# Performance work log

Hardware: AMD Instinct MI355X
Metric: run time of the kernel (lower is better)

## Reference

```python
import jax, jax.numpy as jnp
from jax import lax
import numpy as np

P = 16      # n_latent
T = 16      # n_frames
ALPHA = 0.5


def conv2d(x, w, b):
    # Conv2d(k=3, stride=2, pad=1), NCHW/OIHW
    y = lax.conv_general_dilated(x, w, (2, 2), ((1, 1), (1, 1)),
                                 dimension_numbers=('NCHW', 'OIHW', 'NCHW'))
    return y + b[None, :, None, None]


def convT2d(x, w, b):
    # ConvTranspose2d(k=3, stride=2, pad=1, output_pad=1): lhs_dilation=2,
    # pad low = k-1-p = 1, pad high = k-1-p+op = 2, kernel flipped, I/O swapped.
    wk = jnp.flip(w, (2, 3)).transpose(1, 0, 2, 3)
    y = lax.conv_general_dilated(x, wk, (1, 1), ((1, 2), (1, 2)),
                                 lhs_dilation=(2, 2),
                                 dimension_numbers=('NCHW', 'OIHW', 'NCHW'))
    return y + b[None, :, None, None]


def build_tridiag(D, Boff, alpha):
    # D: [B, P*P*T], Boff: [B, P*P*(T-1)] -> block-tridiagonal [B, P*T, P*T]
    b = D.shape[0]
    Db = D.reshape(b, T, P, P)
    Bb = Boff.reshape(b, T - 1, P, P)
    blocks = jnp.zeros((b, T, T, P, P), D.dtype)
    i = jnp.arange(T)
    blocks = blocks.at[:, i, i].set(Db)                                # diagonal blocks
    blocks = blocks.at[:, i[1:], i[:-1]].set(Bb)                        # sub-diagonal
    blocks = blocks.at[:, i[:-1], i[1:]].set(Bb.transpose(0, 1, 3, 2))  # super-diagonal (transposed)
    M = blocks.transpose(0, 1, 3, 2, 4).reshape(b, P * T, P * T)
    return M + alpha * jnp.eye(P * T, dtype=D.dtype)


def setup_inputs() -> dict:
    key = jax.random.key(0)
    ks = jax.random.split(key, 20)
    B = 256

    def kaiming(k, shape, fan_in):
        return jax.random.normal(k, shape, jnp.float32) * np.float32(np.sqrt(2.0 / fan_in))

    inp = {}
    inp['x'] = jax.random.normal(ks[0], (B, T, 32, 32), jnp.float32)
    inp['eps'] = jax.random.normal(ks[1], (B, P * T), jnp.float32)
    # encoder convs
    inp['w1'] = kaiming(ks[2], (32, 1, 3, 3), 9);     inp['b1'] = jnp.zeros((32,), jnp.float32)
    inp['w2'] = kaiming(ks[3], (32, 32, 3, 3), 288);  inp['b2'] = jnp.zeros((32,), jnp.float32)
    inp['w3'] = kaiming(ks[4], (64, 32, 3, 3), 288);  inp['b3'] = jnp.zeros((64,), jnp.float32)
    inp['w4'] = kaiming(ks[5], (64, 64, 3, 3), 576);  inp['b4'] = jnp.zeros((64,), jnp.float32)
    inp['w5'] = kaiming(ks[6], (64, 64, 3, 3), 576);  inp['b5'] = jnp.zeros((64,), jnp.float32)
    # encoder fc heads
    F = 64 * T
    inp['fc_mu_w'] = kaiming(ks[7], (P * T, F), F);   inp['fc_mu_b'] = jnp.zeros((P * T,), jnp.float32)
    # tiny std so alpha*I dominates -> precision matrix is PD (valid Cholesky)
    inp['fc_D_w'] = jax.random.normal(ks[8], (P * P * T, F), jnp.float32) * np.float32(3e-5)
    inp['fc_D_b'] = jnp.zeros((P * P * T,), jnp.float32)
    inp['fc_B_w'] = jax.random.normal(ks[9], (P * P * (T - 1), F), jnp.float32) * np.float32(3e-5)
    inp['fc_B_b'] = jnp.zeros((P * P * (T - 1),), jnp.float32)
    # decoder
    inp['fc_dec_w'] = kaiming(ks[10], (F, P * T), P * T); inp['fc_dec_b'] = jnp.zeros((F,), jnp.float32)
    inp['wt5'] = kaiming(ks[11], (64, 64, 3, 3), 576); inp['bt5'] = jnp.zeros((64,), jnp.float32)
    inp['wt4'] = kaiming(ks[12], (64, 64, 3, 3), 576); inp['bt4'] = jnp.zeros((64,), jnp.float32)
    inp['wt3'] = kaiming(ks[13], (64, 32, 3, 3), 576); inp['bt3'] = jnp.zeros((32,), jnp.float32)
    inp['wt2'] = kaiming(ks[14], (32, 32, 3, 3), 288); inp['bt2'] = jnp.zeros((32,), jnp.float32)
    inp['wt1'] = kaiming(ks[15], (32, 1, 3, 3), 288);  inp['bt1'] = jnp.zeros((1,), jnp.float32)
    return inp


def reference(x, eps, w1, b1, w2, b2, w3, b3, w4, b4, w5, b5,
              fc_mu_w, fc_mu_b, fc_D_w, fc_D_b, fc_B_w, fc_B_b,
              fc_dec_w, fc_dec_b, wt5, bt5, wt4, bt4, wt3, bt3,
              wt2, bt2, wt1, bt1):
    Bsz = x.shape[0]
    # ---- encode ----
    h = x.reshape(-1, 1, 32, 32)
    for w, b in ((w1, b1), (w2, b2), (w3, b3), (w4, b4), (w5, b5)):
        h = jax.nn.relu(conv2d(h, w, b))      # ends at [B*T, 64, 1, 1]
    h = h.reshape(Bsz, 64 * T)
    mu = h @ fc_mu_w.T + fc_mu_b              # [B, P*T]
    Dv = h @ fc_D_w.T + fc_D_b                # [B, P*P*T]
    Bv = h @ fc_B_w.T + fc_B_b                # [B, P*P*(T-1)]
    # ---- reparametrize ----
    Pm = build_tridiag(Dv, Bv, ALPHA)         # [B, P*T, P*T]
    L = jnp.linalg.cholesky(Pm)               # lower, uses lower triangle (as torch.cholesky)
    cov = jnp.linalg.inv(L)                   # per-sample inverse of Cholesky factor
    z = mu + jnp.einsum('bij,bj->bi', cov, eps)
    # ---- decode ----
    hd = (z @ fc_dec_w.T + fc_dec_b).reshape(-1, 64, 1, 1)
    for w, b in ((wt5, bt5), (wt4, bt4), (wt3, bt3), (wt2, bt2)):
        hd = jax.nn.elu(convT2d(hd, w, b))
    xr = jax.nn.sigmoid(convT2d(hd, wt1, bt1))  # [B*T, 1, 32, 32]
    return (xr, mu, cov, Pm)
```

## Files before the change

### kernel.cpp

```cpp
#include <hip/hip_runtime.h>
#include <cmath>

#define ALPHA 0.5f

__global__ __launch_bounds__(256) void transpose_all8(
    const float* __restrict__ dw5, const float* __restrict__ dw4,
    const float* __restrict__ dw3, const float* __restrict__ dw2,
    const float* __restrict__ ew2, const float* __restrict__ ew3,
    const float* __restrict__ ew4, const float* __restrict__ ew5,
    float* __restrict__ t5, float* __restrict__ t4,
    float* __restrict__ t3, float* __restrict__ t2,
    float* __restrict__ e2, float* __restrict__ e3,
    float* __restrict__ e4, float* __restrict__ e5)
{
    int idx = blockIdx.x * 256 + threadIdx.x;
    if (idx >= 202752) return;
    const float* w; float* t; int CIN, COUT, loc; bool enc = false;
    if (idx < 36864)       { w = dw5; t = t5; CIN = 64; COUT = 64; loc = idx; }
    else if (idx < 73728)  { w = dw4; t = t4; CIN = 64; COUT = 64; loc = idx - 36864; }
    else if (idx < 92160)  { w = dw3; t = t3; CIN = 64; COUT = 32; loc = idx - 73728; }
    else if (idx < 101376) { w = dw2; t = t2; CIN = 32; COUT = 32; loc = idx - 92160; }
    else if (idx < 110592) { w = ew2; t = e2; CIN = 32; COUT = 32; loc = idx - 101376; enc = true; }
    else if (idx < 129024) { w = ew3; t = e3; CIN = 32; COUT = 64; loc = idx - 110592; enc = true; }
    else if (idx < 165888) { w = ew4; t = e4; CIN = 64; COUT = 64; loc = idx - 129024; enc = true; }
    else                   { w = ew5; t = e5; CIN = 64; COUT = 64; loc = idx - 165888; enc = true; }
    int wk = loc % 9; int r = loc / 9; int ci, co;
    if (enc) { ci = r % CIN;  co = r / CIN;  }
    else     { co = r % COUT; ci = r / COUT; }
    t[wk * CIN * COUT + ci * COUT + co] = w[loc];
}

__device__ __forceinline__ int a1map(int iy, int col) {
    return (col & 7)
         | ((iy & 2) << 2)
         | (((iy ^ (iy >> 2)) & 1) << 4)
         | ((col & 8) << 2)
         | ((iy & 4) << 4)
         | ((iy & 8) << 4);
}

__global__ __launch_bounds__(256, 4) void enc_fused(
    const float* __restrict__ x,
    const float* __restrict__ w1,  const float* __restrict__ b1,
    const float* __restrict__ w2t, const float* __restrict__ b2,
    const float* __restrict__ w3t, const float* __restrict__ b3,
    const float* __restrict__ w4t, const float* __restrict__ b4,
    const float* __restrict__ w5t, const float* __restrict__ b5,
    float* __restrict__ hout)
{
    __shared__ __align__(16) float smem[10240];
    float* a1s  = smem;
    float* bse  = smem + 8192;
    float* imgs = bse;
    float* a2s  = bse;
    float* a3s  = smem;
    float* a4s  = smem + 1024;
    float* reds = smem + 1280;

    const int n = blockIdx.x;
    const int tid = threadIdx.x;

    const float* xi = x + n * 1024;
    #pragma unroll
    for (int i = 0; i < 4; i++) {
        int idx = tid + 256 * i;
        int iy = idx >> 5, ix = idx & 31;
        int col = (ix & 1) ? 20 + (ix >> 1) : (ix >> 1);
        imgs[iy * 40 + col] = xi[idx];
    }
    __syncthreads();

    {
        const int oy = tid >> 4, ox = tid & 15;
        float patch[9];
        #pragma unroll
        for (int ky = 0; ky < 3; ky++) {
            const int iy = 2 * oy - 1 + ky;
            #pragma unroll
            for (int kx = 0; kx < 3; kx++) {
                const int ix = 2 * ox - 1 + kx;
                bool v = (iy >= 0) && (ix >= 0);
                int col = (ix & 1) ? 20 + (ix >> 1) : (ix >> 1);
                patch[ky * 3 + kx] = v ? imgs[iy * 40 + col] : 0.f;
            }
        }
        const int ocol = (ox & 1) ? 8 + (ox >> 1) : (ox >> 1);
        const int sidx = a1map(oy, ocol);
        for (int c = 0; c < 32; c++) {
            float acc = b1[c];
            #pragma unroll
            for (int k = 0; k < 9; k++) acc = fmaf(patch[k], w1[c * 9 + k], acc);
            a1s[c * 256 + sidx] = fmaxf(acc, 0.f);
        }
    }
    __syncthreads();

    {
        const int p = tid & 63, oy = p >> 3, ox = p & 7;
        const int c0u = __builtin_amdgcn_readfirstlane(tid >> 6);
        const int cobase = c0u * 8;
        float acc[8];
        #pragma unroll
        for (int r = 0; r < 8; r++) acc[r] = b2[cobase + r];
        int offs[9]; bool val[9];
        #pragma unroll
        for (int ky = 0; ky < 3; ky++) {
            const int iy = 2 * oy - 1 + ky;
            #pragma unroll
            for (int kx = 0; kx < 3; kx++) {
                const int ix = 2 * ox - 1 + kx;
                const bool v = (iy >= 0) && (ix >= 0);
                const int col = (ix & 1) ? 8 + (ix >> 1) : (ix >> 1);
                offs[ky * 3 + kx] = v ? a1map(iy, col) : 0;
                val[ky * 3 + kx] = v;
            }
        }
        for (int ci = 0; ci < 32; ci++) {
            float patch[9];
            #pragma unroll
            for (int k = 0; k < 9; k++)
                patch[k] = val[k] ? a1s[ci * 256 + offs[k]] : 0.f;
            const float* wci = w2t + ci * 32 + cobase;
            #pragma unroll
            for (int k = 0; k < 9; k++) {
                #pragma unroll
                for (int r = 0; r < 8; r++)
                    acc[r] = fmaf(patch[k], wci[k * 1024 + r], acc[r]);
            }
        }
        __syncthreads();
        #pragma unroll
        for (int r = 0; r < 8; r++)
            a2s[(cobase + r) * 64 + p] = fmaxf(acc[r], 0.f);
    }
    __syncthreads();

    {
        const int px = tid & 15, oy = px >> 2, ox = px & 3;
        const int cg = tid >> 4;
        float4 bv = ((const float4*)b3)[cg];
        float acc[4] = {bv.x, bv.y, bv.z, bv.w};
        for (int ci = 0; ci < 32; ci++) {
            float patch[9];
            #pragma unroll
            for (int ky = 0; ky < 3; ky++) {
                const int iy = 2 * oy - 1 + ky;
                #pragma unroll
                for (int kx = 0; kx < 3; kx++) {
                    const int ix = 2 * ox - 1 + kx;
                    bool v = (iy >= 0) && (ix >= 0);
                    patch[ky * 3 + kx] = v ? a2s[ci * 64 + iy * 8 + ix] : 0.f;
                }
            }
            #pragma unroll
            for (int k = 0; k < 9; k++) {
                float4 wv = *(const float4*)(w3t + k * 2048 + ci * 64 + cg * 4);
                acc[0] = fmaf(patch[k], wv.x, acc[0]);
                acc[1] = fmaf(patch[k], wv.y, acc[1]);
                acc[2] = fmaf(patch[k], wv.z, acc[2]);
                acc[3] = fmaf(patch[k], wv.w, acc[3]);
            }
        }
        #pragma unroll
        for (int r = 0; r < 4; r++)
            a3s[(cg * 4 + r) * 16 + px] = fmaxf(acc[r], 0.f);
    }
    __syncthreads();

    {
        const int co = tid & 63;
        const int part = __builtin_amdgcn_readfirstlane(tid >> 6);
        float a0 = 0.f, a1 = 0.f, a2 = 0.f, a3 = 0.f;
        for (int ci = part * 16; ci < part * 16 + 16; ci++) {
            const float* wp = w4t + ci * 64 + co;
            const float w0 = wp[0];
            const float w1 = wp[4096];
            const float w2 = wp[8192];
            const float w3 = wp[12288];
            const float w4 = wp[16384];
            const float w5 = wp[20480];
            const float w6 = wp[24576];
            const float w7 = wp[28672];
            const float w8 = wp[32768];
            const float4 r0 = *(const float4*)(a3s + ci * 16);
            const float4 r1 = *(const float4*)(a3s + ci * 16 + 4);
            const float4 r2 = *(const float4*)(a3s + ci * 16 + 8);
            const float4 r3 = *(const float4*)(a3s + ci * 16 + 12);
            a0 = fmaf(r0.x, w4, a0); a0 = fmaf(r0.y, w5, a0);
            a0 = fmaf(r1.x, w7, a0); a0 = fmaf(r1.y, w8, a0);
            a1 = fmaf(r0.y, w3, a1); a1 = fmaf(r0.z, w4, a1); a1 = fmaf(r0.w, w5, a1);
            a1 = fmaf(r1.y, w6, a1); a1 = fmaf(r1.z, w7, a1); a1 = fmaf(r1.w, w8, a1);
            a2 = fmaf(r1.x, w1, a2); a2 = fmaf(r1.y, w2, a2);
            a2 = fmaf(r2.x, w4, a2); a2 = fmaf(r2.y, w5, a2);
            a2 = fmaf(r3.x, w7, a2); a2 = fmaf(r3.y, w8, a2);
            a3 = fmaf(r1.y, w0, a3); a3 = fmaf(r1.z, w1, a3); a3 = fmaf(r1.w, w2, a3);
            a3 = fmaf(r2.y, w3, a3); a3 = fmaf(r2.z, w4, a3); a3 = fmaf(r2.w, w5, a3);
            a3 = fmaf(r3.y, w6, a3); a3 = fmaf(r3.z, w7, a3); a3 = fmaf(r3.w, w8, a3);
        }
        float* reds2 = bse;
        reds2[part * 256 +   0 + co] = a0;
        reds2[part * 256 +  64 + co] = a1;
        reds2[part * 256 + 128 + co] = a2;
        reds2[part * 256 + 192 + co] = a3;
        __syncthreads();
        {
            const int co2 = tid & 63;
            const int cls2 = __builtin_amdgcn_readfirstlane(tid >> 6);
            float s = b4[co2]
                    + reds2[      cls2 * 64 + co2] + reds2[256 + cls2 * 64 + co2]
                    + reds2[512 + cls2 * 64 + co2] + reds2[768 + cls2 * 64 + co2];
            a4s[co2 * 4 + cls2] = fmaxf(s, 0.f);
        }
    }
    __syncthreads();

    {
        const int c = tid & 63, part = tid >> 6;
        float s = 0.f;
        for (int ci = part * 16; ci < part * 16 + 16; ci++) {
            const float4 av = *(const float4*)(a4s + ci * 4);
            s = fmaf(av.x, w5t[4 * 4096 + ci * 64 + c], s);
            s = fmaf(av.y, w5t[5 * 4096 + ci * 64 + c], s);
            s = fmaf(av.z, w5t[7 * 4096 + ci * 64 + c], s);
            s = fmaf(av.w, w5t[8 * 4096 + ci * 64 + c], s);
        }
        reds[part * 64 + c] = s;
    }
    __syncthreads();
    if (tid < 64) {
        float v = b5[tid] + reds[tid] + reds[64 + tid] + reds[128 + tid] + reds[192 + tid];
        hout[n * 64 + tid] = fmaxf(v, 0.f);
    }
}

__global__ __launch_bounds__(256) void pm_zero(float4* __restrict__ Pm4)
{
    Pm4[blockIdx.x * 256 + threadIdx.x] = make_float4(0.f, 0.f, 0.f, 0.f);
}

__global__ __launch_bounds__(256) void fc_enc(
    const float* __restrict__ h,
    const float* __restrict__ wmu, const float* __restrict__ bmu,
    const float* __restrict__ wD,  const float* __restrict__ bD,
    const float* __restrict__ wB,  const float* __restrict__ bB,
    float* __restrict__ mu, float* __restrict__ Pm)
{
    __shared__ float As[32][65];
    __shared__ float Bs[32][65];
    const int tid = threadIdx.x;
    const int m0 = blockIdx.y * 64;
    const int n0 = blockIdx.x * 64;

    const float* wbase; const float* bias; int nloc; int region;
    if (n0 < 256)       { wbase = wmu; bias = bmu; nloc = n0;        region = 0; }
    else if (n0 < 4352) { wbase = wD;  bias = bD;  nloc = n0 - 256;  region = 1; }
    else                { wbase = wB;  bias = bB;  nloc = n0 - 4352; region = 2; }

    const int tx = tid & 15, ty = tid >> 4;
    float acc[4][4] = {};
    for (int k0 = 0; k0 < 1024; k0 += 32) {
        #pragma unroll
        for (int s = 0; s < 8; s++) {
            int l = tid + 256 * s;
            int row = l >> 5, kk = l & 31;
            As[kk][row] = h[(m0 + row) * 1024 + k0 + kk];
            Bs[kk][row] = wbase[(nloc + row) * 1024 + k0 + kk];
        }
        __syncthreads();
        #pragma unroll
        for (int kk = 0; kk < 32; kk++) {
            float av[4], bv[4];
            #pragma unroll
            for (int i = 0; i < 4; i++) av[i] = As[kk][ty * 4 + i];
            #pragma unroll
            for (int j = 0; j < 4; j++) bv[j] = Bs[kk][tx * 4 + j];
            #pragma unroll
            for (int i = 0; i < 4; i++)
                #pragma unroll
                for (int j = 0; j < 4; j++) acc[i][j] = fmaf(av[i], bv[j], acc[i][j]);
        }
        __syncthreads();
    }
    #pragma unroll
    for (int i = 0; i < 4; i++) {
        int m = m0 + ty * 4 + i;
        size_t pbase = (size_t)m * 65536;
        #pragma unroll
        for (int j = 0; j < 4; j++) {
            int nc = nloc + tx * 4 + j;
            float v = acc[i][j] + bias[nc];
            if (region == 0) {
                mu[m * 256 + nc] = v;
            } else {
                int t = nc >> 8, pi = (nc >> 4) & 15, pj = nc & 15;
                if (region == 1) {
                    int row = t * 16 + pi, col = t * 16 + pj;
                    Pm[pbase + row * 256 + col] = v + (pi == pj ? ALPHA : 0.f);
                } else {
                    int row = (t + 1) * 16 + pi, col = t * 16 + pj;
                    Pm[pbase + row * 256 + col] = v;
                    Pm[pbase + col * 256 + row] = v;
                }
            }
        }
    }
}

__global__ __launch_bounds__(64) void chol_band(
    const float* __restrict__ Pm, float* __restrict__ Lb_g)
{
    __shared__ float Lb[256 * 32 + 32];
    __shared__ float Ds[4096];
    __shared__ float Bs2[3840];
    const int b = blockIdx.x, lane = threadIdx.x;
    const float* Pb = Pm + (size_t)b * 65536;
    for (int i = lane; i < 8224; i += 64) Lb[i] = 0.f;
    for (int i = lane; i < 4096; i += 64) {
        int t = i >> 8, r = (i >> 4) & 15, c = i & 15;
        Ds[i] = Pb[(t * 16 + r) * 256 + t * 16 + c];
    }
    for (int i = lane; i < 3840; i += 64) {
        int t = i >> 8, r = (i >> 4) & 15, c = i & 15;
        Bs2[i] = Pb[((t + 1) * 16 + r) * 256 + t * 16 + c];
    }
    __syncthreads();

    const int d = lane;
    for (int j = 0; j < 256; j++) {
        const int i = j + d;
        float s = 0.f;
        if (d < 32 && i < 256) {
            int bi = i >> 4, bj = j >> 4, pi = i & 15, pj = j & 15;
            float a;
            if (bi == bj)           a = Ds[bi * 256 + pi * 16 + pj];
            else if (bi == bj + 1)  a = Bs2[bj * 256 + pi * 16 + pj];
            else                    a = 0.f;

            float c[32], p[32];
            const float* cp = Lb + j * 32;
            #pragma unroll
            for (int q = 0; q < 8; q++)
                *(float4*)(c + 4 * q) = *(const float4*)(cp + 4 * q);
            const float* pp = Lb + i * 32 + d;
            #pragma unroll
            for (int m = 1; m < 32; m++) p[m] = pp[m];

            float s0 = 0.f, s1 = 0.f, s2 = 0.f, s3 = 0.f;
            #pragma unroll
            for (int m = 1; m <= 28; m += 4) {
                s0 = fmaf(p[m],     c[m],     s0);
                s1 = fmaf(p[m + 1], c[m + 1], s1);
                s2 = fmaf(p[m + 2], c[m + 2], s2);
                s3 = fmaf(p[m + 3], c[m + 3], s3);
            }
            s0 = fmaf(p[29], c[29], s0);
            s1 = fmaf(p[30], c[30], s1);
            s2 = fmaf(p[31], c[31], s2);
            s = a - ((s0 + s1) + (s2 + s3));
        }
        float diag = __shfl(s, 0);
        float Ljj = sqrtf(diag);
        if (d == 0)                  Lb[j * 32] = Ljj;
        else if (d < 32 && i < 256)  Lb[i * 32 + d] = s / Ljj;
        __syncthreads();
    }
    for (int i = lane; i < 8192; i += 64) Lb_g[b * 8192 + i] = Lb[i];
}

__global__ __launch_bounds__(256) void inv_band(
    const float* __restrict__ Lb_g, float* __restrict__ cov)
{
    __shared__ __align__(16) float Ls[8192];
    __shared__ float rs[256];
    const int b = blockIdx.x, j = threadIdx.x;
    float* covb = cov + (size_t)b * 65536;

    {
        const float4* src = (const float4*)(Lb_g + b * 8192);
        float4* dst = (float4*)Ls;
        #pragma unroll
        for (int q = 0; q < 8; q++) dst[j + 256 * q] = src[j + 256 * q];
    }
    __syncthreads();
    rs[j] = 1.f / Ls[j * 32];
    __syncthreads();

    const int w = __builtin_amdgcn_readfirstlane(j >> 6);
    const int istart = w * 64;

    for (int i = 0; i < istart; i++) covb[i * 256 + j] = 0.f;

    float g[32];
    #pragma unroll
    for (int q = 0; q < 32; q++) g[q] = 0.f;

    for (int c = istart; c < 256; c += 32) {
        #pragma unroll
        for (int u = 0; u < 32; u++) {
            const int i = c + u;
            const float* Lr = Ls + i * 32;
            float s0 = 0.f, s1 = 0.f, s2 = 0.f, s3 = 0.f;
            #pragma unroll
            for (int d = 1; d < 32; d += 4) {
                s0 = fmaf(Lr[d],     g[(u - d) & 31],     s0);
                if (d + 1 < 32) s1 = fmaf(Lr[d + 1], g[(u - d - 1) & 31], s1);
                if (d + 2 < 32) s2 = fmaf(Lr[d + 2], g[(u - d - 2) & 31], s2);
                if (d + 3 < 32) s3 = fmaf(Lr[d + 3], g[(u - d - 3) & 31], s3);
            }
            float s = (s0 + s1) + (s2 + s3);
            float gi = (((i == j) ? 1.f : 0.f) - s) * rs[i];
            g[u & 31] = gi;
            covb[i * 256 + j] = gi;
        }
    }
}

__global__ __launch_bounds__(256) void zvec_k(
    const float* __restrict__ cov, const float* __restrict__ mu,
    const float* __restrict__ eps, float* __restrict__ z)
{
    __shared__ float es[256];
    const int b = blockIdx.x, i = threadIdx.x;
    es[i] = eps[b * 256 + i];
    __syncthreads();
    const float4* row = (const float4*)(cov + (size_t)b * 65536 + i * 256);
    float s = 0.f;
    #pragma unroll 8
    for (int k = 0; k < 64; k++) {
        float4 v = row[k];
        s = fmaf(v.x, es[4 * k], s);
        s = fmaf(v.y, es[4 * k + 1], s);
        s = fmaf(v.z, es[4 * k + 2], s);
        s = fmaf(v.w, es[4 * k + 3], s);
    }
    z[b * 256 + i] = mu[b * 256 + i] + s;
}

__global__ __launch_bounds__(256) void fc_dec_k(
    const float* __restrict__ z, const float* __restrict__ w,
    const float* __restrict__ bias, float* __restrict__ hd0)
{
    __shared__ float zs[256];
    const int blk = blockIdx.x;
    const int b = blk >> 2;
    const int f = ((blk & 3) << 8) + threadIdx.x;
    zs[threadIdx.x] = z[b * 256 + threadIdx.x];
    __syncthreads();
    const float4* wr = (const float4*)(w + f * 256);
    float s = 0.f;
    #pragma unroll 8
    for (int k = 0; k < 64; k++) {
        float4 v = wr[k];
        s = fmaf(v.x, zs[4 * k], s);
        s = fmaf(v.y, zs[4 * k + 1], s);
        s = fmaf(v.z, zs[4 * k + 2], s);
        s = fmaf(v.w, zs[4 * k + 3], s);
    }
    hd0[b * 1024 + f] = s + bias[f];
}

__global__ __launch_bounds__(256) void mu_fix(
    const float* __restrict__ h, const float* __restrict__ w,
    const float* __restrict__ bias, float* __restrict__ mu)
{
    __shared__ float hs[1024];
    const int b = blockIdx.x, p = threadIdx.x;
    #pragma unroll
    for (int i = 0; i < 4; i++) hs[p + 256 * i] = h[b * 1024 + p + 256 * i];
    __syncthreads();
    const float4* wr = (const float4*)(w + p * 1024);
    float s = 0.f;
    #pragma unroll 8
    for (int k = 0; k < 256; k++) {
        float4 v = wr[k];
        s = fmaf(v.x, hs[4 * k], s);
        s = fmaf(v.y, hs[4 * k + 1], s);
        s = fmaf(v.z, hs[4 * k + 2], s);
        s = fmaf(v.w, hs[4 * k + 3], s);
    }
    mu[b * 256 + p] = s + bias[p];
}

__device__ __forceinline__ float eluf(float v) { return v > 0.f ? v : expf(v) - 1.f; }

template<int PY, int PX, int HIN, int WIN, class F>
__device__ __forceinline__ void for_taps(int ey, int ex, F&& f) {
    if (PY == 0) {
        if (PX == 0) { f(4, ey, ex, true); }
        else         { f(5, ey, ex, true); f(3, ey, ex + 1, ex + 1 < WIN); }
    } else {
        if (PX == 0) { f(7, ey, ex, true); f(1, ey + 1, ex, ey + 1 < HIN); }
        else {
            f(8, ey, ex, true);
            f(6, ey, ex + 1, ex + 1 < WIN);
            f(2, ey + 1, ex, ey + 1 < HIN);
            f(0, ey + 1, ex + 1, (ey + 1 < HIN) && (ex + 1 < WIN));
        }
    }
}

template<int OY>
__device__ __forceinline__ void t4_row(
    const float* __restrict__ wt4t, const float* __restrict__ bt4,
    const float* __restrict__ d1, float* __restrict__ d2, int co)
{
    float a0 = 0.f, a1 = 0.f, a2 = 0.f, a3 = 0.f;
    const float* wb = wt4t + co;
    for (int ci = 0; ci < 64; ci++) {
        const float* base = d1 + ci * 12;
        if (OY % 2 == 0) {
            float4 r = *(const float4*)(base + (OY / 2) * 4);
            float w10 = wb[3 * 4096 + ci * 64];
            float w11 = wb[4 * 4096 + ci * 64];
            float w12 = wb[5 * 4096 + ci * 64];
            a0 = fmaf(r.x, w11, a0);
            a1 = fmaf(r.x, w12, a1); a1 = fmaf(r.y, w10, a1);
            a2 = fmaf(r.y, w11, a2);
            a3 = fmaf(r.y, w12, a3); a3 = fmaf(r.z, w10, a3);
        } else {
            float4 ra = *(const float4*)(base + ((OY - 1) / 2) * 4);
            float4 rb = *(const float4*)(base + ((OY + 1) / 2) * 4);
            float w20 = wb[6 * 4096 + ci * 64], w21 = wb[7 * 4096 + ci * 64], w22 = wb[8 * 4096 + ci * 64];
            float w00 = wb[0 * 4096 + ci * 64], w01 = wb[1 * 4096 + ci * 64], w02 = wb[2 * 4096 + ci * 64];
            a0 = fmaf(ra.x, w21, a0); a0 = fmaf(rb.x, w01, a0);
            a1 = fmaf(ra.x, w22, a1); a1 = fmaf(ra.y, w20, a1);
            a1 = fmaf(rb.x, w02, a1); a1 = fmaf(rb.y, w00, a1);
            a2 = fmaf(ra.y, w21, a2); a2 = fmaf(rb.y, w01, a2);
            a3 = fmaf(ra.y, w22, a3); a3 = fmaf(ra.z, w20, a3);
            a3 = fmaf(rb.y, w02, a3); a3 = fmaf(rb.z, w00, a3);
        }
    }
    float b = bt4[co];
    float4 o = make_float4(eluf(a0 + b), eluf(a1 + b), eluf(a2 + b), eluf(a3 + b));
    *(float4*)(d2 + co * 44 + OY * 8) = o;
}

template<int M>
__device__ __forceinline__ void xrow(float* acc, const float* R, float w0, float w1, float w2)
{
    #pragma unroll
    for (int m = 0; m < M; m++) {
        acc[2 * m]     = fmaf(R[m], w1, acc[2 * m]);
        acc[2 * m + 1] = fmaf(R[m], w2, acc[2 * m + 1]);
        acc[2 * m + 1] = fmaf(R[m + 1], w0, acc[2 * m + 1]);
    }
}

__global__ __launch_bounds__(256, 4) void dec_fused(
    const float* __restrict__ hd0,
    const float* __restrict__ wt5t, const float* __restrict__ bt5,
    const float* __restrict__ wt4t, const float* __restrict__ bt4,
    const float* __restrict__ wt3t, const float* __restrict__ bt3,
    const float* __restrict__ wt2t, const float* __restrict__ bt2,
    const float* __restrict__ wt1,  const float* __restrict__ bt1,
    float* __restrict__ xr)
{
    __shared__ __align__(16) float smem[9664];
    float* d0  = smem;
    float* d1  = smem + 64;
    float* d2  = smem + 832;
    float* scr = smem + 3648;
    float* d3  = smem + 6208;
    float* d4  = smem;

    const int n = blockIdx.x, tid = threadIdx.x;

    for (int i = tid; i < 3584; i += 256) smem[64 + i] = 0.f;
    for (int i = tid; i < 3456; i += 256) d3[i] = 0.f;
    if (tid < 64) d0[tid] = hd0[n * 64 + tid];
    __syncthreads();

    {
        const int co = tid & 63;
        const int wv = __builtin_amdgcn_readfirstlane(tid >> 6);
        const int oy = wv >> 1, ox = wv & 1;
        const int wk = (oy + 1) * 3 + (ox + 1);
        const float* wp = wt5t + wk * 4096 + co;
        float s = bt5[co];
        for (int ci = 0; ci < 64; ci++)
            s = fmaf(d0[ci], wp[ci * 64], s);
        d1[co * 12 + oy * 4 + ox] = eluf(s);
    }
    __syncthreads();

    {
        const int co = tid & 63;
        const int oyw = __builtin_amdgcn_readfirstlane(tid >> 6);
        if (oyw == 0)      t4_row<0>(wt4t, bt4, d1, d2, co);
        else if (oyw == 1) t4_row<1>(wt4t, bt4, d1, d2, co);
        else if (oyw == 2) t4_row<2>(wt4t, bt4, d1, d2, co);
        else               t4_row<3>(wt4t, bt4, d1, d2, co);
    }
    __syncthreads();

    {
        const int co = tid & 31, pr = (tid >> 5) & 3, cih = tid >> 7;
        const int e = (pr & 1) ? 7 - pr : pr;
        const int o = (pr & 1) ? pr : 7 - pr;
        const int iy_e = e >> 1, iy_o2 = (o - 1) >> 1, iy_o0 = (o + 1) >> 1;
        float acce[8] = {}, acco[8] = {};
        const float* wb = wt3t + co;
        for (int c = 0; c < 32; c++) {
            const int ci = cih * 32 + c;
            const float* base = d2 + ci * 44;
            float re[8], ro2[8], ro0[8];
            *(float4*)(re)      = *(const float4*)(base + iy_e * 8);
            *(float4*)(re + 4)  = *(const float4*)(base + iy_e * 8 + 4);
            *(float4*)(ro2)     = *(const float4*)(base + iy_o2 * 8);
            *(float4*)(ro2 + 4) = *(const float4*)(base + iy_o2 * 8 + 4);
            *(float4*)(ro0)     = *(const float4*)(base + iy_o0 * 8);
            *(float4*)(ro0 + 4) = *(const float4*)(base + iy_o0 * 8 + 4);
            float w10 = wb[3 * 2048 + ci * 32], w11 = wb[4 * 2048 + ci * 32], w12 = wb[5 * 2048 + ci * 32];
            float w20 = wb[6 * 2048 + ci * 32], w21 = wb[7 * 2048 + ci * 32], w22 = wb[8 * 2048 + ci * 32];
            float w00 = wb[0 * 2048 + ci * 32], w01 = wb[1 * 2048 + ci * 32], w02 = wb[2 * 2048 + ci * 32];
            xrow<4>(acce, re, w10, w11, w12);
            xrow<4>(acco, ro2, w20, w21, w22);
            xrow<4>(acco, ro0, w00, w01, w02);
        }
        if (cih == 1) {
            float* s = scr + (tid - 128) * 20;
            #pragma unroll
            for (int k = 0; k < 8; k++) { s[k] = acce[k]; s[8 + k] = acco[k]; }
        }
        __syncthreads();
        if (cih == 0) {
            const float* s = scr + tid * 20;
            const float b = bt3[co];
            float* oe = d3 + co * 108 + e * 12;
            float* oo = d3 + co * 108 + o * 12;
            #pragma unroll
            for (int k = 0; k < 8; k++) {
                oe[k] = eluf(acce[k] + s[k] + b);
                oo[k] = eluf(acco[k] + s[8 + k] + b);
            }
        }
    }
    __syncthreads();

    {
        const int co = tid & 31, org = tid >> 5;
        float acc0[16] = {}, acc1[16] = {};
        const float* wb = wt2t + co;
        for (int ci = 0; ci < 32; ci++) {
            const float* base = d3 + ci * 108 + org * 12;
            float A[12], B[12];
            #pragma unroll
            for (int q = 0; q < 3; q++) {
                *(float4*)(A + 4 * q) = *(const float4*)(base + 4 * q);
                *(float4*)(B + 4 * q) = *(const float4*)(base + 12 + 4 * q);
            }
            float w10 = wb[3 * 1024 + ci * 32], w11 = wb[4 * 1024 + ci * 32], w12 = wb[5 * 1024 + ci * 32];
            float w20 = wb[6 * 1024 + ci * 32], w21 = wb[7 * 1024 + ci * 32], w22 = wb[8 * 1024 + ci * 32];
            float w00 = wb[0 * 1024 + ci * 32], w01 = wb[1 * 1024 + ci * 32], w02 = wb[2 * 1024 + ci * 32];
            xrow<8>(acc0, A, w10, w11, w12);
            xrow<8>(acc1, A, w20, w21, w22);
            xrow<8>(acc1, B, w00, w01, w02);
        }
        __syncthreads();
        const float b = bt2[co];
        float* o0 = d4 + co * 260 + (2 * org) * 16;
        float* o1 = o0 + 16;
        #pragma unroll
        for (int q = 0; q < 4; q++) {
            float4 v0 = make_float4(eluf(acc0[4 * q] + b), eluf(acc0[4 * q + 1] + b),
                                    eluf(acc0[4 * q + 2] + b), eluf(acc0[4 * q + 3] + b));
            float4 v1 = make_float4(eluf(acc1[4 * q] + b), eluf(acc1[4 * q + 1] + b),
                                    eluf(acc1[4 * q + 2] + b), eluf(acc1[4 * q + 3] + b));
            *(float4*)(o0 + 4 * q) = v0;
            *(float4*)(o1 + 4 * q) = v1;
        }
    }
    __syncthreads();

    {
        const int ey = tid >> 4, ex = tid & 15;
        const float bb = bt1[0];
        float* xi = xr + n * 1024;
        float acc[4] = {};
        for (int ci = 0; ci < 32; ci++) {
            const float* a = d4 + ci * 260;
            const float* w = wt1 + ci * 9;
            for_taps<0, 0, 16, 16>(ey, ex, [&](int wk, int iy, int ix, bool v) {
                acc[0] = fmaf(v ? a[iy * 16 + ix] : 0.f, w[wk], acc[0]); });
            for_taps<0, 1, 16, 16>(ey, ex, [&](int wk, int iy, int ix, bool v) {
                acc[1] = fmaf(v ? a[iy * 16 + ix] : 0.f, w[wk], acc[1]); });
            for_taps<1, 0, 16, 16>(ey, ex, [&](int wk, int iy, int ix, bool v) {
                acc[2] = fmaf(v ? a[iy * 16 + ix] : 0.f, w[wk], acc[2]); });
            for_taps<1, 1, 16, 16>(ey, ex, [&](int wk, int iy, int ix, bool v) {
                acc[3] = fmaf(v ? a[iy * 16 + ix] : 0.f, w[wk], acc[3]); });
        }
        xi[(2 * ey) * 32 + 2 * ex]         = 1.f / (1.f + expf(-(acc[0] + bb)));
        xi[(2 * ey) * 32 + 2 * ex + 1]     = 1.f / (1.f + expf(-(acc[1] + bb)));
        xi[(2 * ey + 1) * 32 + 2 * ex]     = 1.f / (1.f + expf(-(acc[2] + bb)));
        xi[(2 * ey + 1) * 32 + 2 * ex + 1] = 1.f / (1.f + expf(-(acc[3] + bb)));
    }
}

extern "C" void kernel_launch(void* const* d_in, const int* in_sizes, int n_in,
                              void* d_out, int out_size, void* d_ws, size_t ws_size,
                              hipStream_t stream)
{
    (void)in_sizes; (void)n_in; (void)out_size; (void)ws_size;
    const float* x    = (const float*)d_in[0];
    const float* eps  = (const float*)d_in[1];
    const float* w1 = (const float*)d_in[2];  const float* b1 = (const float*)d_in[3];
    const float* w2 = (const float*)d_in[4];  const float* b2 = (const float*)d_in[5];
    const float* w3 = (const float*)d_in[6];  const float* b3 = (const float*)d_in[7];
    const float* w4 = (const float*)d_in[8];  const float* b4 = (const float*)d_in[9];
    const float* w5 = (const float*)d_in[10]; const float* b5 = (const float*)d_in[11];
    const float* fc_mu_w = (const float*)d_in[12]; const float* fc_mu_b = (const float*)d_in[13];
    const float* fc_D_w  = (const float*)d_in[14]; const float* fc_D_b  = (const float*)d_in[15];
    const float* fc_B_w  = (const float*)d_in[16]; const float* fc_B_b  = (const float*)d_in[17];
    const float* fc_dec_w = (const float*)d_in[18]; const float* fc_dec_b = (const float*)d_in[19];
    const float* wt5 = (const float*)d_in[20]; const float* bt5 = (const float*)d_in[21];
    const float* wt4 = (const float*)d_in[22]; const float* bt4 = (const float*)d_in[23];
    const float* wt3 = (const float*)d_in[24]; const float* bt3 = (const float*)d_in[25];
    const float* wt2 = (const float*)d_in[26]; const float* bt2 = (const float*)d_in[27];
    const float* wt1 = (const float*)d_in[28]; const float* bt1 = (const float*)d_in[29];

    float* ws   = (float*)d_ws;
    float* h    = ws;
    float* Lb   = ws + 262144;
    float* z    = ws + 2359296;
    float* hd0  = ws + 2424832;
    float* wt5t = ws + 2686976;
    float* wt4t = ws + 2723840;
    float* wt3t = ws + 2760704;
    float* wt2t = ws + 2779136;
    float* w2t  = ws + 2788352;
    float* w3t  = ws + 2797568;
    float* w4t  = ws + 2816000;
    float* w5t  = ws + 2852864;

    float* out = (float*)d_out;
    float* xr  = out;
    float* mu  = out + 4194304;
    float* cov = out + 4259840;
    float* Pm  = out + 21037056;

    transpose_all8<<<792, 256, 0, stream>>>(wt5, wt4, wt3, wt2, w2, w3, w4, w5,
                                            wt5t, wt4t, wt3t, wt2t, w2t, w3t, w4t, w5t);
    enc_fused<<<4096, 256, 0, stream>>>(x, w1, b1, w2t, b2, w3t, b3, w4t, b4, w5t, b5, h);
    pm_zero<<<16384, 256, 0, stream>>>((float4*)Pm);
    fc_enc<<<dim3(128, 4), 256, 0, stream>>>(h, fc_mu_w, fc_mu_b, fc_D_w, fc_D_b,
                                             fc_B_w, fc_B_b, mu, Pm);
    chol_band<<<256, 64, 0, stream>>>(Pm, Lb);
    inv_band<<<256, 256, 0, stream>>>(Lb, cov);
    zvec_k<<<256, 256, 0, stream>>>(cov, mu, eps, z);
    fc_dec_k<<<1024, 256, 0, stream>>>(z, fc_dec_w, fc_dec_b, hd0);
    dec_fused<<<4096, 256, 0, stream>>>(hd0, wt5t, bt5, wt4t, bt4, wt3t, bt3,
                                        wt2t, bt2, wt1, bt1, xr);
    mu_fix<<<256, 256, 0, stream>>>(h, fc_mu_w, fc_mu_b, mu);
}
```

Before: 977.5 us.

## Merge zero-fill into prep kernel, fuse fc_dec with mu, vectorize inner loops

After: 992.7 us. No clear change (+1.6%).

```diff
diff --git a/kernel.cpp b/kernel.cpp
--- a/kernel.cpp
+++ b/kernel.cpp
@@ -3,7 +3,7 @@
 
 #define ALPHA 0.5f
 
-__global__ __launch_bounds__(256) void transpose_all8(
+__global__ __launch_bounds__(256) void prep_all(
     const float* __restrict__ dw5, const float* __restrict__ dw4,
     const float* __restrict__ dw3, const float* __restrict__ dw2,
     const float* __restrict__ ew2, const float* __restrict__ ew3,
@@ -11,9 +11,15 @@
     float* __restrict__ t5, float* __restrict__ t4,
     float* __restrict__ t3, float* __restrict__ t2,
     float* __restrict__ e2, float* __restrict__ e3,
-    float* __restrict__ e4, float* __restrict__ e5)
-{
-    int idx = blockIdx.x * 256 + threadIdx.x;
+    float* __restrict__ e4, float* __restrict__ e5,
+    float4* __restrict__ Pm4)
+{
+    const int bid = blockIdx.x;
+    if (bid < 16384) {
+        Pm4[bid * 256 + threadIdx.x] = make_float4(0.f, 0.f, 0.f, 0.f);
+        return;
+    }
+    int idx = (bid - 16384) * 256 + threadIdx.x;
     if (idx >= 202752) return;
     const float* w; float* t; int CIN, COUT, loc; bool enc = false;
     if (idx < 36864)       { w = dw5; t = t5; CIN = 64; COUT = 64; loc = idx; }
@@ -233,11 +239,6 @@
     }
 }
 
-__global__ __launch_bounds__(256) void pm_zero(float4* __restrict__ Pm4)
-{
-    Pm4[blockIdx.x * 256 + threadIdx.x] = make_float4(0.f, 0.f, 0.f, 0.f);
-}
-
 __global__ __launch_bounds__(256) void fc_enc(
     const float* __restrict__ h,
     const float* __restrict__ wmu, const float* __restrict__ bmu,
@@ -399,13 +400,17 @@
         for (int u = 0; u < 32; u++) {
             const int i = c + u;
             const float* Lr = Ls + i * 32;
+            float lrow[32];
+            #pragma unroll
+            for (int q = 0; q < 8; q++)
+                *(float4*)(lrow + 4 * q) = *(const float4*)(Lr + 4 * q);
             float s0 = 0.f, s1 = 0.f, s2 = 0.f, s3 = 0.f;
             #pragma unroll
             for (int d = 1; d < 32; d += 4) {
-                s0 = fmaf(Lr[d],     g[(u - d) & 31],     s0);
-                if (d + 1 < 32) s1 = fmaf(Lr[d + 1], g[(u - d - 1) & 31], s1);
-                if (d + 2 < 32) s2 = fmaf(Lr[d + 2], g[(u - d - 2) & 31], s2);
-                if (d + 3 < 32) s3 = fmaf(Lr[d + 3], g[(u - d - 3) & 31], s3);
+                s0 = fmaf(lrow[d],     g[(u - d) & 31],     s0);
+                if (d + 1 < 32) s1 = fmaf(lrow[d + 1], g[(u - d - 1) & 31], s1);
+                if (d + 2 < 32) s2 = fmaf(lrow[d + 2], g[(u - d - 2) & 31], s2);
+                if (d + 3 < 32) s3 = fmaf(lrow[d + 3], g[(u - d - 3) & 31], s3);
             }
             float s = (s0 + s1) + (s2 + s3);
             float gi = (((i == j) ? 1.f : 0.f) - s) * rs[i];
@@ -436,68 +441,50 @@
     z[b * 256 + i] = mu[b * 256 + i] + s;
 }
 
-__global__ __launch_bounds__(256) void fc_dec_k(
+__global__ __launch_bounds__(256) void fc_dec_mu(
     const float* __restrict__ z, const float* __restrict__ w,
-    const float* __restrict__ bias, float* __restrict__ hd0)
-{
-    __shared__ float zs[256];
+    const float* __restrict__ bias, float* __restrict__ hd0,
+    const float* __restrict__ h, const float* __restrict__ wmu,
+    const float* __restrict__ bmu, float* __restrict__ mu)
+{
+    __shared__ float sh[1024];
     const int blk = blockIdx.x;
-    const int b = blk >> 2;
-    const int f = ((blk & 3) << 8) + threadIdx.x;
-    zs[threadIdx.x] = z[b * 256 + threadIdx.x];
-    __syncthreads();
-    const float4* wr = (const float4*)(w + f * 256);
-    float s = 0.f;
-    #pragma unroll 8
-    for (int k = 0; k < 64; k++) {
-        float4 v = wr[k];
-        s = fmaf(v.x, zs[4 * k], s);
-        s = fmaf(v.y, zs[4 * k + 1], s);
-        s = fmaf(v.z, zs[4 * k + 2], s);
-        s = fmaf(v.w, zs[4 * k + 3], s);
-    }
-    hd0[b * 1024 + f] = s + bias[f];
-}
-
-__global__ __launch_bounds__(256) void mu_fix(
-    const float* __restrict__ h, const float* __restrict__ w,
-    const float* __restrict__ bias, float* __restrict__ mu)
-{
-    __shared__ float hs[1024];
-    const int b = blockIdx.x, p = threadIdx.x;
-    #pragma unroll
-    for (int i = 0; i < 4; i++) hs[p + 256 * i] = h[b * 1024 + p + 256 * i];
-    __syncthreads();
-    const float4* wr = (const float4*)(w + p * 1024);
-    float s = 0.f;
-    #pragma unroll 8
-    for (int k = 0; k < 256; k++) {
-        float4 v = wr[k];
-        s = fmaf(v.x, hs[4 * k], s);
-        s = fmaf(v.y, hs[4 * k + 1], s);
-        s = fmaf(v.z, hs[4 * k + 2], s);
-        s = fmaf(v.w, hs[4 * k + 3], s);
-    }
-    mu[b * 256 + p] = s + bias[p];
+    if (blk < 1024) {
+        const int b = blk >> 2;
+        const int f = ((blk & 3) << 8) + threadIdx.x;
+        sh[threadIdx.x] = z[b * 256 + threadIdx.x];
+        __syncthreads();
+        const float4* wr = (const float4*)(w + f * 256);
+        float s = 0.f;
+        #pragma unroll 8
+        for (int k = 0; k < 64; k++) {
+            float4 v = wr[k];
+            s = fmaf(v.x, sh[4 * k], s);
+            s = fmaf(v.y, sh[4 * k + 1], s);
+            s = fmaf(v.z, sh[4 * k + 2], s);
+            s = fmaf(v.w, sh[4 * k + 3], s);
+        }
+        hd0[b * 1024 + f] = s + bias[f];
+    } else {
+        const int b = blk - 1024, p = threadIdx.x;
+        #pragma unroll
+        for (int i = 0; i < 4; i++) sh[p + 256 * i] = h[b * 1024 + p + 256 * i];
+        __syncthreads();
+        const float4* wr = (const float4*)(wmu + p * 1024);
+        float s = 0.f;
+        #pragma unroll 8
+        for (int k = 0; k < 256; k++) {
+            float4 v = wr[k];
+            s = fmaf(v.x, sh[4 * k], s);
+            s = fmaf(v.y, sh[4 * k + 1], s);
+            s = fmaf(v.z, sh[4 * k + 2], s);
+            s = fmaf(v.w, sh[4 * k + 3], s);
+        }
+        mu[b * 256 + p] = s + bmu[p];
+    }
 }
 
 __device__ __forceinline__ float eluf(float v) { return v > 0.f ? v : expf(v) - 1.f; }
-
-template<int PY, int PX, int HIN, int WIN, class F>
-__device__ __forceinline__ void for_taps(int ey, int ex, F&& f) {
-    if (PY == 0) {
-        if (PX == 0) { f(4, ey, ex, true); }
-        else         { f(5, ey, ex, true); f(3, ey, ex + 1, ex + 1 < WIN); }
-    } else {
-        if (PX == 0) { f(7, ey, ex, true); f(1, ey + 1, ex, ey + 1 < HIN); }
-        else {
-            f(8, ey, ex, true);
-            f(6, ey, ex + 1, ex + 1 < WIN);
-            f(2, ey + 1, ex, ey + 1 < HIN);
-            f(0, ey + 1, ex + 1, (ey + 1 < HIN) && (ex + 1 < WIN));
-        }
-    }
-}
 
 template<int OY>
 __device__ __forceinline__ void t4_row(
@@ -577,8 +564,14 @@
         const int wk = (oy + 1) * 3 + (ox + 1);
         const float* wp = wt5t + wk * 4096 + co;
         float s = bt5[co];
-        for (int ci = 0; ci < 64; ci++)
-            s = fmaf(d0[ci], wp[ci * 64], s);
+        #pragma unroll
+        for (int q = 0; q < 16; q++) {
+            float4 dv = *(const float4*)(d0 + 4 * q);
+            s = fmaf(dv.x, wp[(4 * q) * 64], s);
+            s = fmaf(dv.y, wp[(4 * q + 1) * 64], s);
+            s = fmaf(dv.z, wp[(4 * q + 2) * 64], s);
+            s = fmaf(dv.w, wp[(4 * q + 3) * 64], s);
+        }
         d1[co * 12 + oy * 4 + ox] = eluf(s);
     }
     __syncthreads();
@@ -674,20 +667,26 @@
 
     {
         const int ey = tid >> 4, ex = tid & 15;
+        const bool vx = (ex + 1) < 16, vy = (ey + 1) < 16;
         const float bb = bt1[0];
         float* xi = xr + n * 1024;
         float acc[4] = {};
         for (int ci = 0; ci < 32; ci++) {
             const float* a = d4 + ci * 260;
             const float* w = wt1 + ci * 9;
-            for_taps<0, 0, 16, 16>(ey, ex, [&](int wk, int iy, int ix, bool v) {
-                acc[0] = fmaf(v ? a[iy * 16 + ix] : 0.f, w[wk], acc[0]); });
-            for_taps<0, 1, 16, 16>(ey, ex, [&](int wk, int iy, int ix, bool v) {
-                acc[1] = fmaf(v ? a[iy * 16 + ix] : 0.f, w[wk], acc[1]); });
-            for_taps<1, 0, 16, 16>(ey, ex, [&](int wk, int iy, int ix, bool v) {
-                acc[2] = fmaf(v ? a[iy * 16 + ix] : 0.f, w[wk], acc[2]); });
-            for_taps<1, 1, 16, 16>(ey, ex, [&](int wk, int iy, int ix, bool v) {
-                acc[3] = fmaf(v ? a[iy * 16 + ix] : 0.f, w[wk], acc[3]); });
+            const float v00 = a[ey * 16 + ex];
+            const float v01 = vx ? a[ey * 16 + ex + 1] : 0.f;
+            const float v10 = vy ? a[(ey + 1) * 16 + ex] : 0.f;
+            const float v11 = (vx && vy) ? a[(ey + 1) * 16 + ex + 1] : 0.f;
+            acc[0] = fmaf(v00, w[4], acc[0]);
+            acc[1] = fmaf(v00, w[5], acc[1]);
+            acc[1] = fmaf(v01, w[3], acc[1]);
+            acc[2] = fmaf(v00, w[7], acc[2]);
+            acc[2] = fmaf(v10, w[1], acc[2]);
+            acc[3] = fmaf(v00, w[8], acc[3]);
+            acc[3] = fmaf(v01, w[6], acc[3]);
+            acc[3] = fmaf(v10, w[2], acc[3]);
+            acc[3] = fmaf(v11, w[0], acc[3]);
         }
         xi[(2 * ey) * 32 + 2 * ex]         = 1.f / (1.f + expf(-(acc[0] + bb)));
         xi[(2 * ey) * 32 + 2 * ex + 1]     = 1.f / (1.f + expf(-(acc[1] + bb)));
@@ -738,17 +737,17 @@
     float* cov = out + 4259840;
     float* Pm  = out + 21037056;
 
-    transpose_all8<<<792, 256, 0, stream>>>(wt5, wt4, wt3, wt2, w2, w3, w4, w5,
-                                            wt5t, wt4t, wt3t, wt2t, w2t, w3t, w4t, w5t);
+    prep_all<<<17176, 256, 0, stream>>>(wt5, wt4, wt3, wt2, w2, w3, w4, w5,
+                                        wt5t, wt4t, wt3t, wt2t, w2t, w3t, w4t, w5t,
+                                        (float4*)Pm);
     enc_fused<<<4096, 256, 0, stream>>>(x, w1, b1, w2t, b2, w3t, b3, w4t, b4, w5t, b5, h);
-    pm_zero<<<16384, 256, 0, stream>>>((float4*)Pm);
     fc_enc<<<dim3(128, 4), 256, 0, stream>>>(h, fc_mu_w, fc_mu_b, fc_D_w, fc_D_b,
                                              fc_B_w, fc_B_b, mu, Pm);
     chol_band<<<256, 64, 0, stream>>>(Pm, Lb);
     inv_band<<<256, 256, 0, stream>>>(Lb, cov);
     zvec_k<<<256, 256, 0, stream>>>(cov, mu, eps, z);
-    fc_dec_k<<<1024, 256, 0, stream>>>(z, fc_dec_w, fc_dec_b, hd0);
+    fc_dec_mu<<<1280, 256, 0, stream>>>(z, fc_dec_w, fc_dec_b, hd0,
+                                        h, fc_mu_w, fc_mu_b, mu);
     dec_fused<<<4096, 256, 0, stream>>>(hd0, wt5t, bt5, wt4t, bt4, wt3t, bt3,
                                         wt2t, bt2, wt1, bt1, xr);
-    mu_fix<<<256, 256, 0, stream>>>(h, fc_mu_w, fc_mu_b, mu);
-}
+}
```
